# Optimization experiments

Measured on AMD Instinct MI355X. Metric: run time of the kernel, lower is better.

Reference implementation:

```python
import jax, jax.numpy as jnp
import numpy as np

B, T, D = 2, 2048, 512
H = 8
DH = D // H
DECAY = 0.99
SCALE = DH ** -0.5
NEG = -1e30

_J6 = jnp.array([[0, 0, 0, 0, 0, 1], [0, 0, 0, 0, -1, 0], [0, 0, 0, 1, 0, 0],
                 [0, 0, 1, 0, 0, 0], [0, -1, 0, 0, 0, 0], [1, 0, 0, 0, 0, 0]],
                dtype=jnp.float32)
_PAIRS4 = [(0, 1), (0, 2), (0, 3), (1, 2), (1, 3), (2, 3)]


def exterior(p1, p2):
    # p1, p2: [..., 4] -> normalized Plucker line coords [..., 6]
    parts = [p1[..., i] * p2[..., j] - p1[..., j] * p2[..., i] for i, j in _PAIRS4]
    L = jnp.stack(parts, axis=-1)
    n = jnp.sqrt(jnp.sum(L * L, axis=-1, keepdims=True))
    return L / jnp.maximum(n, 1e-12)


def setup_inputs() -> dict:
    key = jax.random.key(0)
    ks = jax.random.split(key, 16)
    s = 0.02
    return {
        "x": jax.random.normal(ks[0], (B, T, D), jnp.float32),
        "qkv_w": jax.random.normal(ks[1], (3 * D, D), jnp.float32) * s,
        "qkv_b": jnp.zeros((3 * D,), jnp.float32),
        "w1_write": jax.random.normal(ks[2], (4 * H, D), jnp.float32) * s,
        "w2_write": jax.random.normal(ks[3], (4 * H, D), jnp.float32) * s,
        "w1_read": jax.random.normal(ks[4], (4 * H, D), jnp.float32) * s,
        "w2_read": jax.random.normal(ks[5], (4 * H, D), jnp.float32) * s,
        "mem_value_w": jax.random.normal(ks[6], (D, D), jnp.float32) * s,
        "mem_value_b": jnp.zeros((D,), jnp.float32),
        "mem_gate_w": jax.random.normal(ks[7], (H, D), jnp.float32) * s,
        "mem_gate_b": jnp.zeros((H,), jnp.float32),
        "mem_scale": jnp.full((H,), 0.1, jnp.float32),
        "out_w": jax.random.normal(ks[8], (D, D), jnp.float32) * s,
        "out_b": jnp.zeros((D,), jnp.float32),
    }


def reference(x, qkv_w, qkv_b, w1_write, w2_write, w1_read, w2_read,
              mem_value_w, mem_value_b, mem_gate_w, mem_gate_b, mem_scale,
              out_w, out_b):
    b, t, d = x.shape
    # --- standard causal attention (dropout in eval mode = identity) ---
    qkv = (x @ qkv_w.T + qkv_b).reshape(b, t, 3, H, DH)
    qkv = jnp.transpose(qkv, (2, 0, 3, 1, 4))  # [3,B,H,T,dh]
    q, k, v = qkv[0], qkv[1], qkv[2]
    scores = jnp.einsum('bhtd,bhsd->bhts', q, k) * SCALE
    i = jnp.arange(t)
    upper = i[:, None] < i[None, :]  # strictly upper -> masked
    scores = jnp.where(upper, NEG, scores)
    attn = jax.nn.softmax(scores, axis=-1)
    seq_out = jnp.einsum('bhts,bhsd->bhtd', attn, v)
    seq_out = jnp.transpose(seq_out, (0, 2, 1, 3)).reshape(b, t, d)
    # --- exterior-algebra Gram memory ---
    x_prev = jnp.concatenate([jnp.zeros((b, 1, d), x.dtype), x[:, :-1]], axis=1)
    w1 = (x_prev @ w1_write.T).reshape(b, t, H, 4)
    w2 = (x @ w2_write.T).reshape(b, t, H, 4)
    write_lines = exterior(w1, w2)  # [B,T,H,6]
    r1 = (x @ w1_read.T).reshape(b, t, H, 4)
    r2 = (x @ w2_read.T).reshape(b, t, H, 4)
    read_lines = exterior(r1, r2)  # [B,T,H,6]
    J_write = jnp.einsum('bthi,ij->bthj', write_lines, _J6)
    # incidence[b,h,i,j] = <read_i, J write_j>
    incidence = jnp.einsum('bihk,bjhk->bhij', read_lines, J_write)  # [B,H,T,T]
    # decay weights, strictly lower triangular (j < i); also acts as causal mask
    pos = jnp.arange(t, dtype=x.dtype)
    delta = pos[:, None] - pos[None, :]
    weights = jnp.where(delta > 0, jnp.power(jnp.asarray(DECAY, x.dtype), delta), 0.0)
    mem_score = jnp.sum((incidence * incidence) * weights[None, None], axis=-1)  # [B,H,T]
    # --- gating ---
    mem_val = x @ mem_value_w.T + mem_value_b  # [B,T,D]
    gate = jax.nn.sigmoid(x @ mem_gate_w.T + mem_gate_b)  # [B,T,H]
    mem_score_t = jnp.transpose(mem_score, (0, 2, 1))  # [B,T,H]
    gated = jax.nn.sigmoid(mem_score_t * mem_scale[None, None, :]) * gate
    gated = jnp.mean(gated, axis=-1, keepdims=True)  # [B,T,1]
    return (seq_out + gated * mem_val) @ out_w.T + out_b
```

## Files before the change

### kernel.cpp

```cpp
#include <hip/hip_runtime.h>
#include <math.h>

#define B_ 2
#define T_ 2048
#define D_ 512
#define H_ 8
#define DH_ 64
#define SCALE_ 0.125f
#define DECAY_ 0.99f

static constexpr size_t QSZ = (size_t)B_ * H_ * T_ * DH_;

typedef __bf16 bf16x8 __attribute__((ext_vector_type(8)));
typedef float f32x4 __attribute__((ext_vector_type(4)));

__device__ inline ushort f2bf(float f) {
  uint u = __float_as_uint(f);
  u += 0x7FFF + ((u >> 16) & 1);
  return (ushort)(u >> 16);
}

__device__ inline float bf2f(ushort v) {
  return __uint_as_float(((uint)v) << 16);
}

__device__ __forceinline__ void gload16(const ushort* g, ushort* l) {
  __builtin_amdgcn_global_load_lds(
      (const __attribute__((address_space(1))) void*)g,
      (__attribute__((address_space(3))) void*)l, 16, 0, 0);
}

__device__ __forceinline__ uint cvtpk(float lo, float hi) {
  uint r;
  asm("v_cvt_pk_bf16_f32 %0, %1, %2" : "=v"(r) : "v"(lo), "v"(hi));
  return r;
}

__global__ __launch_bounds__(256) void cast_bf16_kernel(
    const float* __restrict__ x, const float* __restrict__ qkvw,
    const float* __restrict__ mvw, const float* __restrict__ ow,
    const float* __restrict__ w1w, const float* __restrict__ w2w,
    const float* __restrict__ w1r, const float* __restrict__ w2r,
    const float* __restrict__ mgw, ushort* __restrict__ dst)
{
  size_t e0 = ((size_t)blockIdx.x * 256 + threadIdx.x) * 8;
  const float* src = nullptr;
  if (e0 < 2097152)      src = x + e0;
  else if (e0 < 2883584) src = qkvw + (e0 - 2097152);
  else if (e0 < 3145728) src = mvw + (e0 - 2883584);
  else if (e0 < 3276800) {
    size_t off = e0 - 3145728;
    int row = (int)(off >> 9), col = (int)(off & 511);
    if (row < 32)       src = w1w + (size_t)row * 512 + col;
    else if (row < 64)  src = w2w + (size_t)(row - 32) * 512 + col;
    else if (row < 96)  src = w1r + (size_t)(row - 64) * 512 + col;
    else if (row < 128) src = w2r + (size_t)(row - 96) * 512 + col;
    else if (row < 136) src = mgw + (size_t)(row - 128) * 512 + col;
    else src = nullptr;
  } else if (e0 < 3538944) src = ow + (e0 - 3276800);
  ushort tmp[8];
  if (src) {
    float4 a = *(const float4*)(src);
    float4 b = *(const float4*)(src + 4);
    tmp[0] = f2bf(a.x); tmp[1] = f2bf(a.y); tmp[2] = f2bf(a.z); tmp[3] = f2bf(a.w);
    tmp[4] = f2bf(b.x); tmp[5] = f2bf(b.y); tmp[6] = f2bf(b.z); tmp[7] = f2bf(b.w);
  } else {
#pragma unroll
    for (int i = 0; i < 8; i++) tmp[i] = 0;
  }
  *(uint4*)(dst + e0) = *(uint4*)tmp;
}

template<int EPI>
__global__ __launch_bounds__(256) void mfma_gemm(const ushort* __restrict__ A,
    const ushort* __restrict__ W, const float* __restrict__ bias,
    const float* __restrict__ bias2, void* __restrict__ Cout,
    ushort* __restrict__ memval16, float* __restrict__ proj, int M, int N, int K)
{
  __shared__ __align__(16) ushort As[128 * 64];
  __shared__ __align__(16) ushort Ws[64 * 64];
  const int tid = threadIdx.x;
  const int wave = tid >> 6, lane = tid & 63;
  const int col16 = lane & 15, grp = lane >> 4;
  const int wr = wave >> 1, wc = wave & 1;
  const int gx = gridDim.x;
  const int nwg = gx * gridDim.y;
  const int p = blockIdx.y * gx + blockIdx.x;
  const int wg = (p & 7) * (nwg >> 3) + (p >> 3);
  const int bm = (wg / gx) * 128, bn = (wg % gx) * 64;

  f32x4 acc[4][2] = {};
  const int lrow = lane >> 3, lcol = (lane & 7) * 8;

  for (int k0 = 0; k0 < K; k0 += 64) {
    __syncthreads();
#pragma unroll
    for (int i = 0; i < 4; i++) {
      int q = i * 4 + wave;
      gload16(A + (size_t)(bm + q * 8 + lrow) * K + k0 + lcol, &As[q * 512]);
    }
#pragma unroll
    for (int i = 0; i < 2; i++) {
      int q = i * 4 + wave;
      gload16(W + (size_t)(bn + q * 8 + lrow) * K + k0 + lcol, &Ws[q * 512]);
    }
    __syncthreads();
#pragma unroll
    for (int kk = 0; kk < 2; kk++) {
      bf16x8 a[4], b[2];
#pragma unroll
      for (int m = 0; m < 4; m++)
        a[m] = *(const bf16x8*)&As[(wr * 64 + m * 16 + col16) * 64 + kk * 32 + grp * 8];
#pragma unroll
      for (int n = 0; n < 2; n++)
        b[n] = *(const bf16x8*)&Ws[(wc * 32 + n * 16 + col16) * 64 + kk * 32 + grp * 8];
#pragma unroll
      for (int m = 0; m < 4; m++)
#pragma unroll
        for (int n = 0; n < 2; n++)
          acc[m][n] = __builtin_amdgcn_mfma_f32_16x16x32_bf16(a[m], b[n], acc[m][n], 0, 0, 0);
    }
  }

  if (EPI == 1) {
    ushort* q16 = (ushort*)Cout;
    ushort* k16 = q16 + QSZ;
    ushort* vt  = q16 + 2 * QSZ;
    const int sec = bn >> 9;
    if (sec == 2) {
#pragma unroll
      for (int n = 0; n < 2; n++) {
        int col = bn + wc * 32 + n * 16 + col16;
        float bv = bias[col];
        int h = (col >> 6) & 7, dh = col & 63;
#pragma unroll
        for (int m = 0; m < 4; m++) {
          int row0 = bm + wr * 64 + m * 16 + grp * 4;
          int b = row0 >> 11, t0 = row0 & 2047;
          int tq = (t0 & ~63) + ((t0 >> 5) & 1) * 32 + ((t0 >> 2) & 3) * 8
                 + ((t0 >> 4) & 1) * 4;
          ushort tmp4[4];
#pragma unroll
          for (int r = 0; r < 4; r++) tmp4[r] = f2bf(acc[m][n][r] + bv);
          *(uint2*)(vt + ((size_t)(b * H_ + h) * 64 + dh) * T_ + tq) = *(uint2*)tmp4;
        }
      }
    } else {
#pragma unroll
      for (int n = 0; n < 2; n++) {
        int col = bn + wc * 32 + n * 16 + col16;
        float bv;
        if (sec < 2)       bv = bias[col];
        else if (sec == 3) bv = bias2[col - 1536];
        else               bv = 0.f;
        int h = (col >> 6) & 7, dh = col & 63;
#pragma unroll
        for (int m = 0; m < 4; m++) {
#pragma unroll
          for (int r = 0; r < 4; r++) {
            int row = bm + wr * 64 + m * 16 + grp * 4 + r;
            int b = row >> 11, t = row & 2047;
            float val = acc[m][n][r] + bv;
            size_t bh = (size_t)(b * H_ + h);
            if (sec == 0)      q16[(bh * T_ + t) * 64 + dh] = f2bf(val * (SCALE_ * 1.44269504f));
            else if (sec == 1) k16[(bh * T_ + t) * 64 + dh] = f2bf(val);
            else if (sec == 3) memval16[(size_t)row * 512 + (col - 1536)] = f2bf(val);
            else               proj[(size_t)row * 256 + (col - 2048)] = val;
          }
        }
      }
    }
  } else {
    float* C = (float*)Cout;
#pragma unroll
    for (int n = 0; n < 2; n++) {
      int col = bn + wc * 32 + n * 16 + col16;
      float bv = bias[col];
#pragma unroll
      for (int m = 0; m < 4; m++) {
#pragma unroll
        for (int r = 0; r < 4; r++) {
          int row = bm + wr * 64 + m * 16 + grp * 4 + r;
          C[(size_t)row * N + col] = acc[m][n][r] + bv;
        }
      }
    }
  }
}

__global__ __launch_bounds__(256) void lines_kernel(
    const float* __restrict__ proj, const float* __restrict__ gb,
    float* __restrict__ u_out, float* __restrict__ r_out, float* __restrict__ gate_out)
{
  int gid = blockIdx.x * 256 + threadIdx.x;
  int bt = gid >> 3, h = gid & 7;
  int b = bt >> 11, t = bt & 2047;
  const float* pr = proj + (size_t)bt * 256;
  const int pi[6] = {0, 0, 0, 1, 1, 2};
  const int pj[6] = {1, 2, 3, 2, 3, 3};
  float p1[4], p2[4];
#pragma unroll
  for (int e = 0; e < 4; e++) {
    p1[e] = (t == 0) ? 0.f : proj[(size_t)(bt - 1) * 256 + h * 4 + e];
    p2[e] = pr[32 + h * 4 + e];
  }
  float L[6], n2 = 0.f;
#pragma unroll
  for (int e = 0; e < 6; e++) {
    L[e] = p1[pi[e]] * p2[pj[e]] - p1[pj[e]] * p2[pi[e]];
    n2 = fmaf(L[e], L[e], n2);
  }
  float inv = 1.f / fmaxf(sqrtf(n2), 1e-12f);
  size_t base = (((size_t)(b * H_ + h)) * T_ + t) * 6;
  u_out[base + 0] =  L[5] * inv;
  u_out[base + 1] = -L[4] * inv;
  u_out[base + 2] =  L[3] * inv;
  u_out[base + 3] =  L[2] * inv;
  u_out[base + 4] = -L[1] * inv;
  u_out[base + 5] =  L[0] * inv;
#pragma unroll
  for (int e = 0; e < 4; e++) {
    p1[e] = pr[64 + h * 4 + e];
    p2[e] = pr[96 + h * 4 + e];
  }
  n2 = 0.f;
#pragma unroll
  for (int e = 0; e < 6; e++) {
    L[e] = p1[pi[e]] * p2[pj[e]] - p1[pj[e]] * p2[pi[e]];
    n2 = fmaf(L[e], L[e], n2);
  }
  inv = 1.f / fmaxf(sqrtf(n2), 1e-12f);
#pragma unroll
  for (int e = 0; e < 6; e++) r_out[base + e] = L[e] * inv;
  gate_out[(size_t)bt * H_ + h] = 1.f / (1.f + __expf(-(pr[128 + h] + gb[h])));
}

__global__ __launch_bounds__(128) void memscore3_kernel(
    const float* __restrict__ u, const float* __restrict__ r, float* __restrict__ score)
{
  const int bh = blockIdx.x;
  const int c = blockIdx.y;
  const int tid = threadIdx.x;
  const int base = c << 7;
  const int jmax = base + 128;
  __shared__ float us_t[6][2048];
  __shared__ float red[128][25];

  const float* ug = u + (size_t)bh * T_ * 6;
  for (int idx = tid; idx < jmax * 6; idx += 128) {
    int j = idx / 6;
    int cmp = idx - j * 6;
    us_t[cmp][j] = ug[idx];
  }
  __syncthreads();

  float g[21];
#pragma unroll
  for (int q2 = 0; q2 < 21; q2++) g[q2] = 0.f;
  if (c > 0) {
    float w = __powf(DECAY_, (float)(128 - tid));
    const float d128 = 0.27624712f;
    for (int j = base - 128 + tid; j >= 0; j -= 128) {
      float u0 = us_t[0][j], u1 = us_t[1][j], u2 = us_t[2][j];
      float u3 = us_t[3][j], u4 = us_t[4][j], u5 = us_t[5][j];
      float w0 = w * u0, w1 = w * u1, w2 = w * u2, w3 = w * u3, w4 = w * u4;
      g[0] = fmaf(w0, u0, g[0]);  g[1] = fmaf(w0, u1, g[1]);
      g[2] = fmaf(w0, u2, g[2]);  g[3] = fmaf(w0, u3, g[3]);
      g[4] = fmaf(w0, u4, g[4]);  g[5] = fmaf(w0, u5, g[5]);
      g[6] = fmaf(w1, u1, g[6]);  g[7] = fmaf(w1, u2, g[7]);
      g[8] = fmaf(w1, u3, g[8]);  g[9] = fmaf(w1, u4, g[9]);
      g[10] = fmaf(w1, u5, g[10]); g[11] = fmaf(w2, u2, g[11]);
      g[12] = fmaf(w2, u3, g[12]); g[13] = fmaf(w2, u4, g[13]);
      g[14] = fmaf(w2, u5, g[14]); g[15] = fmaf(w3, u3, g[15]);
      g[16] = fmaf(w3, u4, g[16]); g[17] = fmaf(w3, u5, g[17]);
      g[18] = fmaf(w4, u4, g[18]); g[19] = fmaf(w4, u5, g[19]);
      g[20] = fmaf(w * u5, u5, g[20]);
      w *= d128;
    }
  }
#pragma unroll
  for (int q2 = 0; q2 < 21; q2++) red[tid][q2] = g[q2];
  __syncthreads();
  for (int off = 64; off > 0; off >>= 1) {
    if (tid < off) {
#pragma unroll
      for (int q2 = 0; q2 < 21; q2++) red[tid][q2] += red[tid + off][q2];
    }
    __syncthreads();
  }
  float M21[21];
#pragma unroll
  for (int q2 = 0; q2 < 21; q2++) M21[q2] = red[0][q2];

  const int i = base + tid;
  const float* ri = r + ((size_t)bh * T_ + i) * 6;
  float r0 = ri[0], r1 = ri[1], r2 = ri[2], r3 = ri[3], r4 = ri[4], r5 = ri[5];
  float q = M21[0] * r0 * r0 + M21[6] * r1 * r1 + M21[11] * r2 * r2
          + M21[15] * r3 * r3 + M21[18] * r4 * r4 + M21[20] * r5 * r5
          + 2.f * (M21[1] * r0 * r1 + M21[2] * r0 * r2 + M21[3] * r0 * r3
                 + M21[4] * r0 * r4 + M21[5] * r0 * r5 + M21[7] * r1 * r2
                 + M21[8] * r1 * r3 + M21[9] * r1 * r4 + M21[10] * r1 * r5
                 + M21[12] * r2 * r3 + M21[13] * r2 * r4 + M21[14] * r2 * r5
                 + M21[16] * r3 * r4 + M21[17] * r3 * r5 + M21[19] * r4 * r5);
  float wl = __powf(DECAY_, (float)tid);
  float sum = q * wl;
  float w = wl;
  const float invd = 1.0f / DECAY_;
  const int sbound = tid | 63;
  for (int s = 0; s < sbound; ++s) {
    float d = r0 * us_t[0][base + s] + r1 * us_t[1][base + s]
            + r2 * us_t[2][base + s] + r3 * us_t[3][base + s]
            + r4 * us_t[4][base + s] + r5 * us_t[5][base + s];
    if (s < tid) sum = fmaf(w, d * d, sum);
    w *= invd;
  }
  score[(size_t)bh * T_ + i] = sum;
}

__global__ __launch_bounds__(256) void gfac_kernel(
    const float* __restrict__ score, const float* __restrict__ gate,
    const float* __restrict__ mem_scale, float* __restrict__ gfac)
{
  int bt = blockIdx.x * 256 + threadIdx.x;
  int b = bt >> 11, t = bt & 2047;
  float acc = 0.f;
#pragma unroll
  for (int h = 0; h < H_; h++) {
    float ms = score[((size_t)(b * H_ + h)) * T_ + t];
    float sg = 1.f / (1.f + __expf(-ms * mem_scale[h]));
    acc += sg * gate[(size_t)bt * H_ + h];
  }
  gfac[bt] = acc * (1.0f / H_);
}

__global__ __launch_bounds__(256) void attn_v7_kernel(
    const ushort* __restrict__ q16, const ushort* __restrict__ k16,
    const ushort* __restrict__ vtp16, const ushort* __restrict__ memval16,
    const float* __restrict__ gfac, ushort* __restrict__ seqo16)
{
  const int blk = blockIdx.x;
  const int xcd = blk & 7, rank = blk >> 3;
  const int bh = (xcd << 1) | (rank & 1);
  const int rg = 63 - (rank >> 1);
  const int tid = threadIdx.x;
  const int w = tid >> 6, lane = tid & 63;
  const int col16 = lane & 15, grp = lane >> 4;

  __shared__ __align__(16) float comb[3][64][40];

  const int i0 = rg * 32;
  const ushort* qp0 = q16 + ((size_t)bh * T_ + i0 + col16) * 64 + grp * 8;
  bf16x8 aq[2][2];
  aq[0][0] = *(const bf16x8*)(qp0);
  aq[0][1] = *(const bf16x8*)(qp0 + 32);
  aq[1][0] = *(const bf16x8*)(qp0 + 16 * 64);
  aq[1][1] = *(const bf16x8*)(qp0 + 16 * 64 + 32);

  f32x4 ot[2][4] = {};
  float lsum[2] = {0.f, 0.f};

  const ushort* kb = k16 + (size_t)bh * T_ * 64;
  const ushort* vb = vtp16 + (size_t)bh * 64 * T_;

  const int ntiles = (rg >> 1) + 1;
  for (int kt = w; kt < ntiles; kt += 4) {
    const int j0 = kt * 64;
    bf16x8 vf[2][4];
#pragma unroll
    for (int ks = 0; ks < 2; ks++)
#pragma unroll
      for (int n4 = 0; n4 < 4; n4++)
        vf[ks][n4] = *(const bf16x8*)(vb + (size_t)(n4 * 16 + col16) * T_ +
                                      j0 + ks * 32 + grp * 8);
    const bool lastt = (kt == ntiles - 1);
    uint pk[2][4][2];
#pragma unroll
    for (int jt = 0; jt < 4; jt++) {
      const ushort* kp = kb + (size_t)(j0 + jt * 16 + col16) * 64 + grp * 8;
      bf16x8 b0 = *(const bf16x8*)kp;
      bf16x8 b1 = *(const bf16x8*)(kp + 32);
#pragma unroll
      for (int rr = 0; rr < 2; rr++) {
        f32x4 facc = {};
        __builtin_amdgcn_s_setprio(1);
        facc = __builtin_amdgcn_mfma_f32_16x16x32_bf16(b0, aq[rr][0], facc, 0, 0, 0);
        facc = __builtin_amdgcn_mfma_f32_16x16x32_bf16(b1, aq[rr][1], facc, 0, 0, 0);
        __builtin_amdgcn_s_setprio(0);
        const int i = i0 + rr * 16 + col16;
        float p[4];
#pragma unroll
        for (int r = 0; r < 4; r++) {
          int j = j0 + jt * 16 + grp * 4 + r;
          p[r] = (lastt && j > i) ? 0.f : exp2f(facc[r]);
          lsum[rr] += p[r];
        }
        pk[rr][jt][0] = cvtpk(p[0], p[1]);
        pk[rr][jt][1] = cvtpk(p[2], p[3]);
      }
    }
    __builtin_amdgcn_s_setprio(1);
#pragma unroll
    for (int ks = 0; ks < 2; ks++)
#pragma unroll
      for (int rr = 0; rr < 2; rr++) {
        uint pf_u[4] = {pk[rr][2 * ks][0], pk[rr][2 * ks][1],
                        pk[rr][2 * ks + 1][0], pk[rr][2 * ks + 1][1]};
        bf16x8 pf = *(bf16x8*)pf_u;
#pragma unroll
        for (int n4 = 0; n4 < 4; n4++)
          ot[rr][n4] = __builtin_amdgcn_mfma_f32_16x16x32_bf16(vf[ks][n4], pf, ot[rr][n4], 0, 0, 0);
      }
    __builtin_amdgcn_s_setprio(0);
  }

#pragma unroll
  for (int rr = 0; rr < 2; rr++) {
    lsum[rr] += __shfl_xor(lsum[rr], 16);
    lsum[rr] += __shfl_xor(lsum[rr], 32);
  }

  if (w > 0) {
    float* dst = &comb[w - 1][lane][0];
#pragma unroll
    for (int rr = 0; rr < 2; rr++)
#pragma unroll
      for (int n4 = 0; n4 < 4; n4++)
        *(float4*)&dst[(rr * 4 + n4) * 4] = *(float4*)&ot[rr][n4];
    dst[32] = lsum[0];
    dst[33] = lsum[1];
  }
  __syncthreads();
  if (w == 0) {
#pragma unroll
    for (int ww = 0; ww < 3; ww++) {
      const float* src = &comb[ww][lane][0];
#pragma unroll
      for (int rr = 0; rr < 2; rr++)
#pragma unroll
        for (int n4 = 0; n4 < 4; n4++) {
          float4 v = *(const float4*)&src[(rr * 4 + n4) * 4];
          ot[rr][n4][0] += v.x; ot[rr][n4][1] += v.y;
          ot[rr][n4][2] += v.z; ot[rr][n4][3] += v.w;
        }
      lsum[0] += src[32];
      lsum[1] += src[33];
    }
    const int b = bh >> 3, h = bh & 7;
#pragma unroll
    for (int rr = 0; rr < 2; rr++) {
      const int i = i0 + rr * 16 + col16;
      const float inv = 1.f / lsum[rr];
      const float gf = gfac[b * T_ + i];
      const size_t rowbase = ((size_t)(b * T_) + i) * D_ + h * 64 + grp * 4;
#pragma unroll
      for (int n4 = 0; n4 < 4; n4++) {
        ushort tmp4[4];
#pragma unroll
        for (int r = 0; r < 4; r++) {
          float mv = bf2f(memval16[rowbase + n4 * 16 + r]);
          tmp4[r] = f2bf(fmaf(gf, mv, ot[rr][n4][r] * inv));
        }
        *(uint2*)(seqo16 + rowbase + n4 * 16) = *(uint2*)tmp4;
      }
    }
  }
}

extern "C" void kernel_launch(void* const* d_in, const int* in_sizes, int n_in,
                              void* d_out, int out_size, void* d_ws, size_t ws_size,
                              hipStream_t stream) {
  const float* x     = (const float*)d_in[0];
  const float* qkvw  = (const float*)d_in[1];
  const float* qkvb  = (const float*)d_in[2];
  const float* w1w   = (const float*)d_in[3];
  const float* w2w   = (const float*)d_in[4];
  const float* w1r   = (const float*)d_in[5];
  const float* w2r   = (const float*)d_in[6];
  const float* mvw   = (const float*)d_in[7];
  const float* mvb   = (const float*)d_in[8];
  const float* mgw   = (const float*)d_in[9];
  const float* mgb   = (const float*)d_in[10];
  const float* mscl  = (const float*)d_in[11];
  const float* ow    = (const float*)d_in[12];
  const float* ob    = (const float*)d_in[13];
  (void)in_sizes; (void)n_in; (void)out_size; (void)ws_size;

  float* f = (float*)d_ws;
  float* proj   = f;
  float* ul     = proj + 1048576;
  float* rl     = ul + 196608;
  float* gatep  = rl + 196608;
  float* msc    = gatep + 32768;
  float* gfac   = msc + 32768;
  ushort* x16    = (ushort*)(gfac + 4096);
  ushort* wbig16 = x16 + 2097152;
  ushort* ow16   = wbig16 + 1179648;
  ushort* q16    = ow16 + 262144;
  ushort* k16    = q16 + QSZ;
  ushort* vt16   = k16 + QSZ;
  ushort* memval16 = vt16 + QSZ;
  ushort* seqo16 = x16;

  const int M = B_ * T_;

  cast_bf16_kernel<<<dim3(1728), 256, 0, stream>>>(x, qkvw, mvw, ow,
                                                   w1w, w2w, w1r, w2r, mgw, x16);
  mfma_gemm<1><<<dim3(36, 32), 256, 0, stream>>>(x16, wbig16, qkvb, mvb, q16,
                                                 memval16, proj, M, 2304, D_);
  lines_kernel<<<dim3(128), 256, 0, stream>>>(proj, mgb, ul, rl, gatep);
  memscore3_kernel<<<dim3(16, 16), 128, 0, stream>>>(ul, rl, msc);
  gfac_kernel<<<dim3(16), 256, 0, stream>>>(msc, gatep, mscl, gfac);
  attn_v7_kernel<<<dim3(16 * 64), 256, 0, stream>>>(q16, k16, vt16, memval16,
                                                    gfac, seqo16);
  mfma_gemm<0><<<dim3(8, 32), 256, 0, stream>>>(seqo16, ow16, ob, nullptr, d_out,
                                                nullptr, nullptr, M, D_, D_);
}
```

Measured before the change: 111.4 us.

## Fuse memory-score and gate kernels into attention launch with atomic handoff

Result: slower. 191.1 us (+71.6%).

```diff
diff --git a/kernel.cpp b/kernel.cpp
--- a/kernel.cpp
+++ b/kernel.cpp
@@ -190,8 +190,10 @@
 
 __global__ __launch_bounds__(256) void lines_kernel(
     const float* __restrict__ proj, const float* __restrict__ gb,
-    float* __restrict__ u_out, float* __restrict__ r_out, float* __restrict__ gate_out)
+    float* __restrict__ u_out, float* __restrict__ r_out, float* __restrict__ gate_out,
+    uint* __restrict__ sync)
 {
+  if (blockIdx.x == 0 && threadIdx.x == 0) { sync[0] = 0u; sync[1] = 0u; }
   int gid = blockIdx.x * 256 + threadIdx.x;
   int bt = gid >> 3, h = gid & 7;
   int b = bt >> 11, t = bt & 2047;
@@ -235,118 +237,126 @@
   gate_out[(size_t)bt * H_ + h] = 1.f / (1.f + __expf(-(pr[128 + h] + gb[h])));
 }
 
-__global__ __launch_bounds__(128) void memscore3_kernel(
-    const float* __restrict__ u, const float* __restrict__ r, float* __restrict__ score)
-{
-  const int bh = blockIdx.x;
-  const int c = blockIdx.y;
-  const int tid = threadIdx.x;
-  const int base = c << 7;
-  const int jmax = base + 128;
-  __shared__ float us_t[6][2048];
-  __shared__ float red[128][25];
-
-  const float* ug = u + (size_t)bh * T_ * 6;
-  for (int idx = tid; idx < jmax * 6; idx += 128) {
-    int j = idx / 6;
-    int cmp = idx - j * 6;
-    us_t[cmp][j] = ug[idx];
-  }
-  __syncthreads();
-
-  float g[21];
-#pragma unroll
-  for (int q2 = 0; q2 < 21; q2++) g[q2] = 0.f;
-  if (c > 0) {
-    float w = __powf(DECAY_, (float)(128 - tid));
-    const float d128 = 0.27624712f;
-    for (int j = base - 128 + tid; j >= 0; j -= 128) {
-      float u0 = us_t[0][j], u1 = us_t[1][j], u2 = us_t[2][j];
-      float u3 = us_t[3][j], u4 = us_t[4][j], u5 = us_t[5][j];
-      float w0 = w * u0, w1 = w * u1, w2 = w * u2, w3 = w * u3, w4 = w * u4;
-      g[0] = fmaf(w0, u0, g[0]);  g[1] = fmaf(w0, u1, g[1]);
-      g[2] = fmaf(w0, u2, g[2]);  g[3] = fmaf(w0, u3, g[3]);
-      g[4] = fmaf(w0, u4, g[4]);  g[5] = fmaf(w0, u5, g[5]);
-      g[6] = fmaf(w1, u1, g[6]);  g[7] = fmaf(w1, u2, g[7]);
-      g[8] = fmaf(w1, u3, g[8]);  g[9] = fmaf(w1, u4, g[9]);
-      g[10] = fmaf(w1, u5, g[10]); g[11] = fmaf(w2, u2, g[11]);
-      g[12] = fmaf(w2, u3, g[12]); g[13] = fmaf(w2, u4, g[13]);
-      g[14] = fmaf(w2, u5, g[14]); g[15] = fmaf(w3, u3, g[15]);
-      g[16] = fmaf(w3, u4, g[16]); g[17] = fmaf(w3, u5, g[17]);
-      g[18] = fmaf(w4, u4, g[18]); g[19] = fmaf(w4, u5, g[19]);
-      g[20] = fmaf(w * u5, u5, g[20]);
-      w *= d128;
-    }
-  }
-#pragma unroll
-  for (int q2 = 0; q2 < 21; q2++) red[tid][q2] = g[q2];
-  __syncthreads();
-  for (int off = 64; off > 0; off >>= 1) {
-    if (tid < off) {
-#pragma unroll
-      for (int q2 = 0; q2 < 21; q2++) red[tid][q2] += red[tid + off][q2];
-    }
-    __syncthreads();
-  }
-  float M21[21];
-#pragma unroll
-  for (int q2 = 0; q2 < 21; q2++) M21[q2] = red[0][q2];
-
-  const int i = base + tid;
-  const float* ri = r + ((size_t)bh * T_ + i) * 6;
-  float r0 = ri[0], r1 = ri[1], r2 = ri[2], r3 = ri[3], r4 = ri[4], r5 = ri[5];
-  float q = M21[0] * r0 * r0 + M21[6] * r1 * r1 + M21[11] * r2 * r2
-          + M21[15] * r3 * r3 + M21[18] * r4 * r4 + M21[20] * r5 * r5
-          + 2.f * (M21[1] * r0 * r1 + M21[2] * r0 * r2 + M21[3] * r0 * r3
-                 + M21[4] * r0 * r4 + M21[5] * r0 * r5 + M21[7] * r1 * r2
-                 + M21[8] * r1 * r3 + M21[9] * r1 * r4 + M21[10] * r1 * r5
-                 + M21[12] * r2 * r3 + M21[13] * r2 * r4 + M21[14] * r2 * r5
-                 + M21[16] * r3 * r4 + M21[17] * r3 * r5 + M21[19] * r4 * r5);
-  float wl = __powf(DECAY_, (float)tid);
-  float sum = q * wl;
-  float w = wl;
-  const float invd = 1.0f / DECAY_;
-  const int sbound = tid | 63;
-  for (int s = 0; s < sbound; ++s) {
-    float d = r0 * us_t[0][base + s] + r1 * us_t[1][base + s]
-            + r2 * us_t[2][base + s] + r3 * us_t[3][base + s]
-            + r4 * us_t[4][base + s] + r5 * us_t[5][base + s];
-    if (s < tid) sum = fmaf(w, d * d, sum);
-    w *= invd;
-  }
-  score[(size_t)bh * T_ + i] = sum;
-}
-
-__global__ __launch_bounds__(256) void gfac_kernel(
-    const float* __restrict__ score, const float* __restrict__ gate,
-    const float* __restrict__ mem_scale, float* __restrict__ gfac)
-{
-  int bt = blockIdx.x * 256 + threadIdx.x;
-  int b = bt >> 11, t = bt & 2047;
-  float acc = 0.f;
-#pragma unroll
-  for (int h = 0; h < H_; h++) {
-    float ms = score[((size_t)(b * H_ + h)) * T_ + t];
-    float sg = 1.f / (1.f + __expf(-ms * mem_scale[h]));
-    acc += sg * gate[(size_t)bt * H_ + h];
-  }
-  gfac[bt] = acc * (1.0f / H_);
-}
-
-__global__ __launch_bounds__(256) void attn_v7_kernel(
+__global__ __launch_bounds__(256, 5) void attn_mem_fused(
     const ushort* __restrict__ q16, const ushort* __restrict__ k16,
     const ushort* __restrict__ vtp16, const ushort* __restrict__ memval16,
-    const float* __restrict__ gfac, ushort* __restrict__ seqo16)
+    const float* __restrict__ ul, const float* __restrict__ rl,
+    const float* __restrict__ gatep, const float* __restrict__ mscl,
+    float* __restrict__ msc, float* __restrict__ gfac,
+    uint* __restrict__ sync, ushort* __restrict__ seqo16)
 {
-  const int blk = blockIdx.x;
+  __shared__ __align__(16) float smem[7680];
+  const int tid = threadIdx.x;
+
+  if (blockIdx.x < 256) {
+    const int m = blockIdx.x;
+    const int bh = m >> 4, c = m & 15;
+    const int base = c << 7;
+    float* us_local = smem;
+    float* red = smem + 768;
+    const float* ug = ul + (size_t)bh * T_ * 6;
+    for (int idx = tid; idx < 768; idx += 256) {
+      int jl = idx / 6, cmp = idx - jl * 6;
+      us_local[cmp * 128 + jl] = ug[(size_t)base * 6 + idx];
+    }
+    float g[21];
+#pragma unroll
+    for (int q2 = 0; q2 < 21; q2++) g[q2] = 0.f;
+    if (c > 0 && tid < base) {
+      float w = __powf(DECAY_, (float)(base - tid));
+      const float gr = __powf(DECAY_, -256.0f);
+      for (int j = tid; j < base; j += 256) {
+        const float* uj = ug + (size_t)j * 6;
+        float u0 = uj[0], u1 = uj[1], u2 = uj[2], u3 = uj[3], u4 = uj[4], u5 = uj[5];
+        float w0 = w * u0, w1 = w * u1, w2 = w * u2, w3 = w * u3, w4 = w * u4;
+        g[0] = fmaf(w0, u0, g[0]);  g[1] = fmaf(w0, u1, g[1]);
+        g[2] = fmaf(w0, u2, g[2]);  g[3] = fmaf(w0, u3, g[3]);
+        g[4] = fmaf(w0, u4, g[4]);  g[5] = fmaf(w0, u5, g[5]);
+        g[6] = fmaf(w1, u1, g[6]);  g[7] = fmaf(w1, u2, g[7]);
+        g[8] = fmaf(w1, u3, g[8]);  g[9] = fmaf(w1, u4, g[9]);
+        g[10] = fmaf(w1, u5, g[10]); g[11] = fmaf(w2, u2, g[11]);
+        g[12] = fmaf(w2, u3, g[12]); g[13] = fmaf(w2, u4, g[13]);
+        g[14] = fmaf(w2, u5, g[14]); g[15] = fmaf(w3, u3, g[15]);
+        g[16] = fmaf(w3, u4, g[16]); g[17] = fmaf(w3, u5, g[17]);
+        g[18] = fmaf(w4, u4, g[18]); g[19] = fmaf(w4, u5, g[19]);
+        g[20] = fmaf(w * u5, u5, g[20]);
+        w *= gr;
+      }
+    }
+#pragma unroll
+    for (int q2 = 0; q2 < 21; q2++) red[tid * 25 + q2] = g[q2];
+    __syncthreads();
+    for (int off = 128; off > 0; off >>= 1) {
+      if (tid < off) {
+#pragma unroll
+        for (int q2 = 0; q2 < 21; q2++)
+          red[tid * 25 + q2] += red[(tid + off) * 25 + q2];
+      }
+      __syncthreads();
+    }
+    float M21[21];
+#pragma unroll
+    for (int q2 = 0; q2 < 21; q2++) M21[q2] = red[q2];
+
+    if (tid < 128) {
+      const int i = base + tid;
+      const float* ri = rl + ((size_t)bh * T_ + i) * 6;
+      float r0 = ri[0], r1 = ri[1], r2 = ri[2], r3 = ri[3], r4 = ri[4], r5 = ri[5];
+      float q = M21[0] * r0 * r0 + M21[6] * r1 * r1 + M21[11] * r2 * r2
+              + M21[15] * r3 * r3 + M21[18] * r4 * r4 + M21[20] * r5 * r5
+              + 2.f * (M21[1] * r0 * r1 + M21[2] * r0 * r2 + M21[3] * r0 * r3
+                     + M21[4] * r0 * r4 + M21[5] * r0 * r5 + M21[7] * r1 * r2
+                     + M21[8] * r1 * r3 + M21[9] * r1 * r4 + M21[10] * r1 * r5
+                     + M21[12] * r2 * r3 + M21[13] * r2 * r4 + M21[14] * r2 * r5
+                     + M21[16] * r3 * r4 + M21[17] * r3 * r5 + M21[19] * r4 * r5);
+      float wl = __powf(DECAY_, (float)tid);
+      float sum = q * wl;
+      float w = wl;
+      const float invd = 1.0f / DECAY_;
+      const int sbound = tid | 63;
+      for (int s = 0; s < sbound; ++s) {
+        float d = r0 * us_local[0 * 128 + s] + r1 * us_local[1 * 128 + s]
+                + r2 * us_local[2 * 128 + s] + r3 * us_local[3 * 128 + s]
+                + r4 * us_local[4 * 128 + s] + r5 * us_local[5 * 128 + s];
+        if (s < tid) sum = fmaf(w, d * d, sum);
+        w *= invd;
+      }
+      msc[(size_t)bh * T_ + i] = sum;
+    }
+    __threadfence();
+    __syncthreads();
+    uint* ord_slot = (uint*)(smem + 7168);
+    if (tid == 0)
+      *ord_slot = __hip_atomic_fetch_add(&sync[0], 1u, __ATOMIC_ACQ_REL,
+                                         __HIP_MEMORY_SCOPE_AGENT);
+    __syncthreads();
+    if (*ord_slot == 255u) {
+      __threadfence();
+      for (int bt = tid; bt < B_ * T_; bt += 256) {
+        int b2 = bt >> 11, t2 = bt & 2047;
+        float acc = 0.f;
+#pragma unroll
+        for (int h = 0; h < H_; h++) {
+          float ms2 = msc[((size_t)(b2 * H_ + h)) * T_ + t2];
+          acc += (1.f / (1.f + __expf(-ms2 * mscl[h]))) * gatep[(size_t)bt * H_ + h];
+        }
+        gfac[bt] = acc * (1.0f / H_);
+      }
+      __threadfence();
+      __syncthreads();
+      if (tid == 0)
+        __hip_atomic_store(&sync[1], 1u, __ATOMIC_RELEASE, __HIP_MEMORY_SCOPE_AGENT);
+    }
+    return;
+  }
+
+  const int blk = blockIdx.x - 256;
   const int xcd = blk & 7, rank = blk >> 3;
   const int bh = (xcd << 1) | (rank & 1);
   const int rg = 63 - (rank >> 1);
-  const int tid = threadIdx.x;
   const int w = tid >> 6, lane = tid & 63;
   const int col16 = lane & 15, grp = lane >> 4;
-
-  __shared__ __align__(16) float comb[3][64][40];
+  float (*comb)[64][40] = (float (*)[64][40])smem;
 
   const int i0 = rg * 32;
   const ushort* qp0 = q16 + ((size_t)bh * T_ + i0 + col16) * 64 + grp * 8;
@@ -445,6 +455,9 @@
       lsum[0] += src[32];
       lsum[1] += src[33];
     }
+    while (__hip_atomic_load(&sync[1], __ATOMIC_ACQUIRE,
+                             __HIP_MEMORY_SCOPE_AGENT) == 0u)
+      __builtin_amdgcn_s_sleep(8);
     const int b = bh >> 3, h = bh & 7;
 #pragma unroll
     for (int rr = 0; rr < 2; rr++) {
@@ -492,7 +505,8 @@
   float* gatep  = rl + 196608;
   float* msc    = gatep + 32768;
   float* gfac   = msc + 32768;
-  ushort* x16    = (ushort*)(gfac + 4096);
+  uint*  sync   = (uint*)(gfac + 4096);
+  ushort* x16    = (ushort*)(sync + 16);
   ushort* wbig16 = x16 + 2097152;
   ushort* ow16   = wbig16 + 1179648;
   ushort* q16    = ow16 + 262144;
@@ -507,11 +521,9 @@
                                                    w1w, w2w, w1r, w2r, mgw, x16);
   mfma_gemm<1><<<dim3(36, 32), 256, 0, stream>>>(x16, wbig16, qkvb, mvb, q16,
                                                  memval16, proj, M, 2304, D_);
-  lines_kernel<<<dim3(128), 256, 0, stream>>>(proj, mgb, ul, rl, gatep);
-  memscore3_kernel<<<dim3(16, 16), 128, 0, stream>>>(ul, rl, msc);
-  gfac_kernel<<<dim3(16), 256, 0, stream>>>(msc, gatep, mscl, gfac);
-  attn_v7_kernel<<<dim3(16 * 64), 256, 0, stream>>>(q16, k16, vt16, memval16,
-                                                    gfac, seqo16);
+  lines_kernel<<<dim3(128), 256, 0, stream>>>(proj, mgb, ul, rl, gatep, sync);
+  attn_mem_fused<<<dim3(256 + 16 * 64), 256, 0, stream>>>(
+      q16, k16, vt16, memval16, ul, rl, gatep, mscl, msc, gfac, sync, seqo16);
   mfma_gemm<0><<<dim3(8, 32), 256, 0, stream>>>(seqo16, ow16, ob, nullptr, d_out,
                                                 nullptr, nullptr, M, D_, D_);
 }
```
